# Performance work log

Measured on AMD Instinct MI355X. Metric: run time of the kernel, lower is better.

Reference implementation:

```python
import jax, jax.numpy as jnp
import numpy as np

NUM_FREQS = 10
NUM_VOXELS = 512
N_POINTS = 262144
IN_DIM = 3
INPUT_CH = IN_DIM + 2 * NUM_FREQS * IN_DIM  # 63


def posenc(x, num_freqs):
    # NeRF positional encoding: [x, sin(x*2^0), cos(x*2^0), ..., sin(x*2^(F-1)), cos(x*2^(F-1))]
    freqs = (2.0 ** jnp.arange(num_freqs)).astype(x.dtype)           # (F,)
    xf = x[:, None, :] * freqs[None, :, None]                        # (N, F, D)
    sc = jnp.stack([jnp.sin(xf), jnp.cos(xf)], axis=2)               # (N, F, 2, D)
    return jnp.concatenate([x, sc.reshape(x.shape[0], -1)], axis=-1)  # (N, D + 2*F*D)


def setup_inputs() -> dict:
    key = jax.random.key(0)
    k_x, k_w, k_v = jax.random.split(key, 3)
    X = jax.random.normal(k_x, (N_POINTS, IN_DIM), dtype=jnp.float32)
    # linear_mappings reshaped to (3*num_voxels, input_ch), used as Linear weight (no bias)
    W = jax.random.normal(k_w, (3 * NUM_VOXELS, INPUT_CH), dtype=jnp.float32) * 0.02
    row_ids = jnp.arange(N_POINTS, dtype=jnp.int64 if jax.config.jax_enable_x64 else jnp.int32)
    voxel_ids = jax.random.randint(k_v, (N_POINTS,), 0, NUM_VOXELS)
    return {"X": X, "W": W, "row_ids": row_ids, "voxel_ids": voxel_ids}


def reference(X, W, row_ids, voxel_ids):
    encoded_X = posenc(X, NUM_FREQS)                      # (N, 63)
    rgb_clusters = encoded_X @ W.T                        # (N, 3*num_voxels) -- wasteful dense GEMM
    # col_indices per selected row: [3v, 3v+1, 3v+2]
    cols = jnp.stack([3 * voxel_ids, 3 * voxel_ids + 1, 3 * voxel_ids + 2], axis=1)  # (M, 3)
    vals = rgb_clusters[row_ids[:, None], cols]           # (M, 3)
    rgb = jnp.zeros((X.shape[0], 3), dtype=X.dtype)
    rgb = rgb.at[row_ids].set(vals)
    return rgb
```

## Files before the change

### kernel.cpp

```cpp
#include <hip/hip_runtime.h>
#include <math.h>

#define N_POINTS   262144
#define NUM_FREQS  10
#define NUM_VOXELS 512


typedef _Float16 half2v __attribute__((ext_vector_type(2)));

__device__ __forceinline__ half2v u2h(unsigned int u) {
    union { unsigned int u; half2v h; } c; c.u = u; return c.h;
}

__device__ __forceinline__ float dot2acc(half2v a, half2v b, float acc) {
#if __has_builtin(__builtin_amdgcn_fdot2)
    return __builtin_amdgcn_fdot2(a, b, acc, false);
#else
    return acc + (float)a[0] * (float)b[0] + (float)a[1] * (float)b[1];
#endif
}

__device__ __forceinline__ half2v pkrtz(float a, float b) {
#if __has_builtin(__builtin_amdgcn_cvt_pkrtz)
    auto r = __builtin_amdgcn_cvt_pkrtz(a, b);
    union { decltype(r) r_; half2v h; } c; c.r_ = r; return c.h;
#else
    half2v h; h[0] = (_Float16)a; h[1] = (_Float16)b; return h;
#endif
}

__global__ __launch_bounds__(256) void pack_w(
    const float* __restrict__ W, _Float16* __restrict__ Wp)
{
    const int gid = blockIdx.x * 256 + threadIdx.x;
    const int v   = gid / 48;
    const int e4  = gid % 48;
    const int row = e4 >> 4;
    const int g   = e4 & 15;
    union { _Float16 h[4]; float2 f2; } u;
    #pragma unroll
    for (int j = 0; j < 4; ++j) {
        const int pc = 4 * g + j;
        float val = 0.0f;
        if (pc != 3) {
            const int wc = pc - (pc >= 4);
            val = W[v * 189 + row * 63 + wc];
        }
        u.h[j] = (_Float16)val;
    }
    *reinterpret_cast<float2*>(Wp + (size_t)v * 192 + row * 64 + 4 * g) = u.f2;
}

__device__ __forceinline__ void posenc_pack_dot(
    float x0, float x1, float x2, const _Float16* __restrict__ Wp, int v,
    float& a0, float& a1, float& a2)
{
    half2v eh[32];
    eh[0] = pkrtz(x0, x1);
    eh[1] = pkrtz(x2, 0.0f);

    float s0, c0, s1, c1, s2, c2;
    __sincosf(x0, &s0, &c0);
    __sincosf(x1, &s1, &c1);
    __sincosf(x2, &s2, &c2);
    #pragma unroll
    for (int f = 0; f < NUM_FREQS; ++f) {
        const int b = 2 + 3 * f;
        eh[b + 0] = pkrtz(s0, s1);
        eh[b + 1] = pkrtz(s2, c0);
        eh[b + 2] = pkrtz(c1, c2);
        if (f < NUM_FREQS - 1) {
            const float ns0 = 2.0f*s0*c0, nc0 = c0*c0 - s0*s0;
            const float ns1 = 2.0f*s1*c1, nc1 = c1*c1 - s1*s1;
            const float ns2 = 2.0f*s2*c2, nc2 = c2*c2 - s2*s2;
            s0 = ns0; c0 = nc0; s1 = ns1; c1 = nc1; s2 = ns2; c2 = nc2;
        }
    }

    const uint4* __restrict__ wb = (const uint4*)(Wp + (size_t)v * 192);
    float acc[3];
    #pragma unroll
    for (int r = 0; r < 3; ++r) {
        float a = 0.0f;
        #pragma unroll
        for (int k = 0; k < 8; ++k) {
            const uint4 q = wb[r * 8 + k];
            a = dot2acc(u2h(q.x), eh[4*k + 0], a);
            a = dot2acc(u2h(q.y), eh[4*k + 1], a);
            a = dot2acc(u2h(q.z), eh[4*k + 2], a);
            a = dot2acc(u2h(q.w), eh[4*k + 3], a);
        }
        acc[r] = a;
    }
    a0 = acc[0]; a1 = acc[1]; a2 = acc[2];
}

__global__ __launch_bounds__(512, 4) void voxlin_fused(
    const float* __restrict__ X,
    const _Float16* __restrict__ Wp,
    const int* __restrict__ row_ids,
    const int* __restrict__ voxel_ids,
    float* __restrict__ out)
{
    __shared__ float4 pts[512];
    __shared__ int    hist[NUM_VOXELS];
    __shared__ int    cur[NUM_VOXELS];
    __shared__ int    wsum[8];

    const int t    = threadIdx.x;
    const int lane = t & 63;
    const int wid  = t >> 6;
    const int i    = blockIdx.x * 512 + t;

    const int   v  = voxel_ids[i];
    const float x0 = X[3*i + 0];
    const float x1 = X[3*i + 1];
    const float x2 = X[3*i + 2];
    const int   r  = row_ids[i];

    hist[t] = 0;
    __syncthreads();
    atomicAdd(&hist[v], 1);
    __syncthreads();

    const int c = hist[t];
    int incl = c;
    #pragma unroll
    for (int d = 1; d < 64; d <<= 1) {
        int n = __shfl_up(incl, d);
        if (lane >= d) incl += n;
    }
    if (lane == 63) wsum[wid] = incl;
    __syncthreads();

    int s8 = (lane < 8) ? wsum[lane] : 0;
    #pragma unroll
    for (int d = 1; d < 8; d <<= 1) {
        int n = __shfl_up(s8, d);
        if (lane >= d) s8 += n;
    }
    int ce = __shfl(s8, (wid == 0) ? 0 : (wid - 1));
    if (wid == 0) ce = 0;

    cur[t] = ce + incl - c;
    __syncthreads();

    const int mypos = atomicAdd(&cur[v], 1);
    pts[mypos] = make_float4(x0, x1, x2, __int_as_float(v));
    __syncthreads();

    const float4 q  = pts[t];
    const int    sv = __float_as_int(q.w);
    float a0, a1, a2;
    posenc_pack_dot(q.x, q.y, q.z, Wp, sv, a0, a1, a2);

    pts[t] = make_float4(a0, a1, a2, 0.0f);
    __syncthreads();

    const float4 res = pts[mypos];
    out[3*r + 0] = res.x;
    out[3*r + 1] = res.y;
    out[3*r + 2] = res.z;
}

__global__ __launch_bounds__(256) void voxlin_fallback(
    const float* __restrict__ X, const float* __restrict__ W,
    const int* __restrict__ row_ids, const int* __restrict__ voxel_ids,
    float* __restrict__ out)
{
    const int i = blockIdx.x * 256 + threadIdx.x;
    if (i >= N_POINTS) return;
    const float x0 = X[3*i], x1 = X[3*i+1], x2 = X[3*i+2];
    const int v = voxel_ids[i];
    const float* __restrict__ w0 = W + v * 189;
    const float* __restrict__ w1 = w0 + 63;
    const float* __restrict__ w2 = w0 + 126;
    float a0 = x0*w0[0] + x1*w0[1] + x2*w0[2];
    float a1 = x0*w1[0] + x1*w1[1] + x2*w1[2];
    float a2 = x0*w2[0] + x1*w2[1] + x2*w2[2];
    float s0, c0, s1, c1, s2, c2;
    __sincosf(x0, &s0, &c0); __sincosf(x1, &s1, &c1); __sincosf(x2, &s2, &c2);
    #pragma unroll
    for (int f = 0; f < NUM_FREQS; ++f) {
        const int b = 3 + 6*f;
        a0 += s0*w0[b] + s1*w0[b+1] + s2*w0[b+2] + c0*w0[b+3] + c1*w0[b+4] + c2*w0[b+5];
        a1 += s0*w1[b] + s1*w1[b+1] + s2*w1[b+2] + c0*w1[b+3] + c1*w1[b+4] + c2*w1[b+5];
        a2 += s0*w2[b] + s1*w2[b+1] + s2*w2[b+2] + c0*w2[b+3] + c1*w2[b+4] + c2*w2[b+5];
        if (f < NUM_FREQS - 1) {
            const float ns0 = 2.0f*s0*c0, nc0 = c0*c0 - s0*s0;
            const float ns1 = 2.0f*s1*c1, nc1 = c1*c1 - s1*s1;
            const float ns2 = 2.0f*s2*c2, nc2 = c2*c2 - s2*s2;
            s0 = ns0; c0 = nc0; s1 = ns1; c1 = nc1; s2 = ns2; c2 = nc2;
        }
    }
    const int rr = row_ids[i];
    out[3*rr] = a0; out[3*rr+1] = a1; out[3*rr+2] = a2;
}

extern "C" void kernel_launch(void* const* d_in, const int* in_sizes, int n_in,
                              void* d_out, int out_size, void* d_ws, size_t ws_size,
                              hipStream_t stream) {
    const float* X         = (const float*)d_in[0];
    const float* W         = (const float*)d_in[1];
    const int*   row_ids   = (const int*)d_in[2];
    const int*   voxel_ids = (const int*)d_in[3];
    float*       out       = (float*)d_out;

    const size_t need = (size_t)NUM_VOXELS * 192 * sizeof(_Float16);

    if (ws_size >= need) {
        _Float16* Wp = (_Float16*)d_ws;
        pack_w<<<96, 256, 0, stream>>>(W, Wp);
        voxlin_fused<<<512, 512, 0, stream>>>(X, Wp, row_ids, voxel_ids, out);
    } else {
        voxlin_fallback<<<(N_POINTS + 255) / 256, 256, 0, stream>>>(X, W, row_ids, voxel_ids, out);
    }
}
```

Before: 73.06 us.

## Replace per-block shared sort with global per-voxel bucketing and per-voxel compute

Result: slower. 151.4 us (+107.2%).

```diff
diff --git a/kernel.cpp b/kernel.cpp
--- a/kernel.cpp
+++ b/kernel.cpp
@@ -4,6 +4,7 @@
 #define N_POINTS   262144
 #define NUM_FREQS  10
 #define NUM_VOXELS 512
+#define CAP        2048
 
 
 typedef _Float16 half2v __attribute__((ext_vector_type(2)));
@@ -27,28 +28,6 @@
 #else
     half2v h; h[0] = (_Float16)a; h[1] = (_Float16)b; return h;
 #endif
-}
-
-__global__ __launch_bounds__(256) void pack_w(
-    const float* __restrict__ W, _Float16* __restrict__ Wp)
-{
-    const int gid = blockIdx.x * 256 + threadIdx.x;
-    const int v   = gid / 48;
-    const int e4  = gid % 48;
-    const int row = e4 >> 4;
-    const int g   = e4 & 15;
-    union { _Float16 h[4]; float2 f2; } u;
-    #pragma unroll
-    for (int j = 0; j < 4; ++j) {
-        const int pc = 4 * g + j;
-        float val = 0.0f;
-        if (pc != 3) {
-            const int wc = pc - (pc >= 4);
-            val = W[v * 189 + row * 63 + wc];
-        }
-        u.h[j] = (_Float16)val;
-    }
-    *reinterpret_cast<float2*>(Wp + (size_t)v * 192 + row * 64 + 4 * g) = u.f2;
 }
 
 __device__ __forceinline__ void posenc_pack_dot(
@@ -95,72 +74,64 @@
     a0 = acc[0]; a1 = acc[1]; a2 = acc[2];
 }
 
-__global__ __launch_bounds__(512, 4) void voxlin_fused(
-    const float* __restrict__ X,
-    const _Float16* __restrict__ Wp,
-    const int* __restrict__ row_ids,
-    const int* __restrict__ voxel_ids,
-    float* __restrict__ out)
+__global__ __launch_bounds__(512) void pack_scatter(
+    const float* __restrict__ X, const float* __restrict__ W,
+    const int* __restrict__ row_ids, const int* __restrict__ voxel_ids,
+    _Float16* __restrict__ Wp, int* __restrict__ cur,
+    float4* __restrict__ sorted)
 {
-    __shared__ float4 pts[512];
-    __shared__ int    hist[NUM_VOXELS];
-    __shared__ int    cur[NUM_VOXELS];
-    __shared__ int    wsum[8];
+    const int b = blockIdx.x;
+    if (b >= 512) {
+        const int gid = (b - 512) * 512 + threadIdx.x;
+        const int v   = gid / 48;
+        const int e4  = gid % 48;
+        const int row = e4 >> 4;
+        const int g   = e4 & 15;
+        union { _Float16 h[4]; float2 f2; } u;
+        #pragma unroll
+        for (int j = 0; j < 4; ++j) {
+            const int pc = 4 * g + j;
+            float val = 0.0f;
+            if (pc != 3) {
+                const int wc = pc - (pc >= 4);
+                val = W[v * 189 + row * 63 + wc];
+            }
+            u.h[j] = (_Float16)val;
+        }
+        *reinterpret_cast<float2*>(Wp + (size_t)v * 192 + row * 64 + 4 * g) = u.f2;
+        return;
+    }
 
-    const int t    = threadIdx.x;
-    const int lane = t & 63;
-    const int wid  = t >> 6;
-    const int i    = blockIdx.x * 512 + t;
-
-    const int   v  = voxel_ids[i];
+    const int i  = b * 512 + threadIdx.x;
+    const int v  = voxel_ids[i];
     const float x0 = X[3*i + 0];
     const float x1 = X[3*i + 1];
     const float x2 = X[3*i + 2];
-    const int   r  = row_ids[i];
+    const int r  = row_ids[i];
+    const int pos = atomicAdd(&cur[v], 1);
+    if (pos < CAP)
+        sorted[(size_t)v * CAP + pos] =
+            make_float4(x0, x1, x2, __int_as_float(r));
+}
 
-    hist[t] = 0;
-    __syncthreads();
-    atomicAdd(&hist[v], 1);
-    __syncthreads();
+__global__ __launch_bounds__(256) void voxel_compute(
+    const _Float16* __restrict__ Wp, const int* __restrict__ cur,
+    const float4* __restrict__ sorted, float* __restrict__ out)
+{
+    const int v = blockIdx.x;
+    int n = cur[v];
+    if (n > CAP) n = CAP;
+    const float4* __restrict__ sp = sorted + (size_t)v * CAP;
 
-    const int c = hist[t];
-    int incl = c;
-    #pragma unroll
-    for (int d = 1; d < 64; d <<= 1) {
-        int n = __shfl_up(incl, d);
-        if (lane >= d) incl += n;
+    for (int j = threadIdx.x; j < n; j += 256) {
+        const float4 p = sp[j];
+        float a0, a1, a2;
+        posenc_pack_dot(p.x, p.y, p.z, Wp, v, a0, a1, a2);
+        const int r = __float_as_int(p.w);
+        out[3*r + 0] = a0;
+        out[3*r + 1] = a1;
+        out[3*r + 2] = a2;
     }
-    if (lane == 63) wsum[wid] = incl;
-    __syncthreads();
-
-    int s8 = (lane < 8) ? wsum[lane] : 0;
-    #pragma unroll
-    for (int d = 1; d < 8; d <<= 1) {
-        int n = __shfl_up(s8, d);
-        if (lane >= d) s8 += n;
-    }
-    int ce = __shfl(s8, (wid == 0) ? 0 : (wid - 1));
-    if (wid == 0) ce = 0;
-
-    cur[t] = ce + incl - c;
-    __syncthreads();
-
-    const int mypos = atomicAdd(&cur[v], 1);
-    pts[mypos] = make_float4(x0, x1, x2, __int_as_float(v));
-    __syncthreads();
-
-    const float4 q  = pts[t];
-    const int    sv = __float_as_int(q.w);
-    float a0, a1, a2;
-    posenc_pack_dot(q.x, q.y, q.z, Wp, sv, a0, a1, a2);
-
-    pts[t] = make_float4(a0, a1, a2, 0.0f);
-    __syncthreads();
-
-    const float4 res = pts[mypos];
-    out[3*r + 0] = res.x;
-    out[3*r + 1] = res.y;
-    out[3*r + 2] = res.z;
 }
 
 __global__ __launch_bounds__(256) void voxlin_fallback(
@@ -206,13 +177,23 @@
     const int*   voxel_ids = (const int*)d_in[3];
     float*       out       = (float*)d_out;
 
-    const size_t need = (size_t)NUM_VOXELS * 192 * sizeof(_Float16);
+    const size_t OFF_WP     = 0;
+    const size_t OFF_CUR    = 196608;
+    const size_t OFF_SORTED = 262144;
+    const size_t need = OFF_SORTED + (size_t)NUM_VOXELS * CAP * sizeof(float4);
 
     if (ws_size >= need) {
-        _Float16* Wp = (_Float16*)d_ws;
-        pack_w<<<96, 256, 0, stream>>>(W, Wp);
-        voxlin_fused<<<512, 512, 0, stream>>>(X, Wp, row_ids, voxel_ids, out);
+        char* ws = (char*)d_ws;
+        _Float16* Wp     = (_Float16*)(ws + OFF_WP);
+        int*      cur    = (int*)     (ws + OFF_CUR);
+        float4*   sorted = (float4*)  (ws + OFF_SORTED);
+
+        hipMemsetAsync(cur, 0, NUM_VOXELS * sizeof(int), stream);
+        pack_scatter<<<560, 512, 0, stream>>>(X, W, row_ids, voxel_ids,
+                                              Wp, cur, sorted);
+        voxel_compute<<<NUM_VOXELS, 256, 0, stream>>>(Wp, cur, sorted, out);
     } else {
-        voxlin_fallback<<<(N_POINTS + 255) / 256, 256, 0, stream>>>(X, W, row_ids, voxel_ids, out);
+        voxlin_fallback<<<(N_POINTS + 255) / 256, 256, 0, stream>>>(
+            X, W, row_ids, voxel_ids, out);
     }
 }
```
